# Optimization experiments

Measured on AMD Instinct MI355X. Metric: run time of the kernel, lower is better.

## Reference

```python
import jax, jax.numpy as jnp
import numpy as np
from jax import lax

IMG = 256; STRIDE = 16; FH = FW = 16; A = 9
SCALES = (32.0, 64.0, 128.0); RATIOS = (0.5, 1.0, 2.0)
N_PROP = 2000; CROP = 14
C_BB = 64


def _conv(x, w, b, stride=1, pad='SAME'):
    y = lax.conv_general_dilated(x, w, (stride, stride), pad,
                                 dimension_numbers=('NCHW', 'OIHW', 'NCHW'))
    return y + b[None, :, None, None]


def _anchors():
    s = jnp.array(SCALES, jnp.float32); r = jnp.array(RATIOS, jnp.float32)
    sr = jnp.stack(jnp.meshgrid(s, r, indexing='ij'), -1).reshape(-1, 2)  # [A,2]
    ws = sr[:, 0] * jnp.sqrt(sr[:, 1]); hs = sr[:, 0] / jnp.sqrt(sr[:, 1])
    cy = (jnp.arange(FH, dtype=jnp.float32) + 0.5) * STRIDE
    cx = (jnp.arange(FW, dtype=jnp.float32) + 0.5) * STRIDE
    cy, cx = jnp.meshgrid(cy, cx, indexing='ij')
    cy = cy[..., None]; cx = cx[..., None]  # [FH,FW,1]
    return jnp.stack([cx - ws / 2, cy - hs / 2, cx + ws / 2, cy + hs / 2], -1).reshape(-1, 4)


def _decode(deltas, anchors):
    w = anchors[:, 2] - anchors[:, 0]; h = anchors[:, 3] - anchors[:, 1]
    cx = anchors[:, 0] + 0.5 * w; cy = anchors[:, 1] + 0.5 * h
    ncx = cx + deltas[:, 0] * w; ncy = cy + deltas[:, 1] * h
    nw = w * jnp.exp(deltas[:, 2]); nh = h * jnp.exp(deltas[:, 3])
    return jnp.stack([ncx - 0.5 * nw, ncy - 0.5 * nh, ncx + 0.5 * nw, ncy + 0.5 * nh], -1)


def _clip(b):
    lim = jnp.float32(IMG - 1)
    return jnp.stack([jnp.clip(b[:, 0], 0, lim), jnp.clip(b[:, 1], 0, lim),
                      jnp.clip(b[:, 2], 0, lim), jnp.clip(b[:, 3], 0, lim)], -1)


def _nms(boxes, scores, thr):
    # greedy NMS; returns order (desc score) and keep mask in sorted order
    order = jnp.argsort(-scores)
    b = boxes[order]
    area = jnp.maximum(b[:, 2] - b[:, 0], 0) * jnp.maximum(b[:, 3] - b[:, 1], 0)
    xx1 = jnp.maximum(b[:, None, 0], b[None, :, 0]); yy1 = jnp.maximum(b[:, None, 1], b[None, :, 1])
    xx2 = jnp.minimum(b[:, None, 2], b[None, :, 2]); yy2 = jnp.minimum(b[:, None, 3], b[None, :, 3])
    inter = jnp.maximum(xx2 - xx1, 0) * jnp.maximum(yy2 - yy1, 0)
    iou = inter / (area[:, None] + area[None, :] - inter + 1e-8)
    n = boxes.shape[0]; idx = jnp.arange(n)
    def body(i, keep):
        return keep & ~(keep[i] & (iou[i] > thr) & (idx > i))
    keep = lax.fori_loop(0, n, body, jnp.ones(n, dtype=bool))
    return order, keep


def _crop_resize(feat, nboxes):
    # feat [C,FH,FW]; nboxes [N,4] normalized (y1,x1,y2,x2) -> [N,C,CROP,CROP]
    t = jnp.arange(CROP, dtype=jnp.float32) / (CROP - 1)
    def one(bx):
        y1, x1, y2, x2 = bx
        fy = (y1 + (y2 - y1) * t) * (FH - 1)
        fx = (x1 + (x2 - x1) * t) * (FW - 1)
        y0 = jnp.clip(jnp.floor(fy), 0, FH - 1).astype(jnp.int32); y1i = jnp.clip(y0 + 1, 0, FH - 1)
        x0 = jnp.clip(jnp.floor(fx), 0, FW - 1).astype(jnp.int32); x1i = jnp.clip(x0 + 1, 0, FW - 1)
        wy = (fy - y0.astype(fy.dtype))[:, None]   # [CROP,1]
        wx = (fx - x0.astype(fx.dtype))[None, :]   # [1,CROP]
        g = lambda yi, xi: feat[:, yi[:, None], xi[None, :]]  # [C,CROP,CROP]
        top = g(y0, x0) * (1 - wx) + g(y0, x1i) * wx
        bot = g(y1i, x0) * (1 - wx) + g(y1i, x1i) * wx
        return top * (1 - wy) + bot * wy
    return jax.vmap(one)(nboxes)


def _forward(x, w_bb, b_bb, w_rpn, b_rpn, w_cls, b_cls, w_box, b_box,
             w_fc1, b_fc1, w_fc2, b_fc2, w_rcls, b_rcls, w_rbox, b_rbox,
             w_m1, b_m1, w_m2, b_m2):
    anchors = _anchors()
    feat = jax.nn.relu(_conv(x, w_bb, b_bb, stride=STRIDE, pad='VALID'))  # [1,C,16,16]
    h = jax.nn.relu(_conv(feat, w_rpn, b_rpn))
    rpn_logits = _conv(h, w_cls, b_cls)[0].reshape(A, 2, FH, FW).transpose(2, 3, 0, 1).reshape(-1, 2)
    rpn_deltas = _conv(h, w_box, b_box)[0].reshape(A, 4, FH, FW).transpose(2, 3, 0, 1).reshape(-1, 4)
    scores = jax.nn.softmax(rpn_logits, -1)[:, 1]
    boxes = _clip(_decode(rpn_deltas, anchors))
    order, keep = _nms(boxes, scores, 0.5)
    n = boxes.shape[0]
    prio = jnp.where(keep, 0, 1) * n + jnp.arange(n)   # kept first, in score order
    sel = jnp.argsort(prio)[:N_PROP]
    valid = keep[sel]
    proposals = jnp.where(valid[:, None], boxes[order][sel], 0.0)  # [N_PROP,4] xyxy
    nb = jnp.stack([proposals[:, 1], proposals[:, 0], proposals[:, 3], proposals[:, 2]], -1) / (IMG - 1)
    crops = _crop_resize(feat[0], nb)                  # [N_PROP,C,14,14]
    pooled = crops.reshape(N_PROP, C_BB, 7, 2, 7, 2).max(axis=(3, 5))
    flat = pooled.reshape(N_PROP, -1)
    h1 = jax.nn.relu(flat @ w_fc1 + b_fc1)
    h2 = jax.nn.relu(h1 @ w_fc2 + b_fc2)
    rcnn_logits = h2 @ w_rcls + b_rcls                 # [N_PROP,2]
    rcnn_deltas = h2 @ w_rbox + b_rbox                 # [N_PROP,4]
    m = jax.nn.relu(_conv(crops, w_m1, b_m1))
    rcnn_masks = _conv(m, w_m2, b_m2)                  # [N_PROP,1,14,14]
    det_scores = jax.nn.softmax(rcnn_logits, -1)[:, 1]
    dets = _clip(_decode(rcnn_deltas, proposals))
    s2 = jnp.where(valid, det_scores, -1.0)
    order2, keep2 = _nms(dets, s2, 0.3)
    keep2 = keep2 & valid[order2]
    final_dets = jnp.where(keep2[:, None], dets[order2], 0.0)
    final_scores = jnp.where(keep2, det_scores[order2], 0.0)
    final_masks = jax.nn.sigmoid(rcnn_masks[order2][:, 0]) * keep2[:, None, None].astype(crops.dtype)
    return (rpn_logits, rpn_deltas, proposals, anchors, rcnn_logits, rcnn_deltas,
            rcnn_masks, final_dets, final_masks, final_scores, keep2)


def setup_inputs() -> dict:
    key = jax.random.key(0)
    ks = jax.random.split(key, 24)
    rn = lambda k, sh, s: jax.random.normal(k, sh, dtype=jnp.float32) * s
    C = C_BB
    return {
        'x': rn(ks[0], (1, 3, IMG, IMG), 1.0),
        'w_bb': rn(ks[1], (C, 3, STRIDE, STRIDE), 0.03), 'b_bb': jnp.zeros((C,), jnp.float32),
        'w_rpn': rn(ks[2], (C, C, 3, 3), 0.05), 'b_rpn': jnp.zeros((C,), jnp.float32),
        'w_cls': rn(ks[3], (2 * A, C, 1, 1), 0.05), 'b_cls': jnp.zeros((2 * A,), jnp.float32),
        'w_box': rn(ks[4], (4 * A, C, 1, 1), 0.05), 'b_box': jnp.zeros((4 * A,), jnp.float32),
        'w_fc1': rn(ks[5], (C * 7 * 7, 512), 0.02), 'b_fc1': jnp.zeros((512,), jnp.float32),
        'w_fc2': rn(ks[6], (512, 512), 0.04), 'b_fc2': jnp.zeros((512,), jnp.float32),
        'w_rcls': rn(ks[7], (512, 2), 0.05), 'b_rcls': jnp.zeros((2,), jnp.float32),
        'w_rbox': rn(ks[8], (512, 4), 0.05), 'b_rbox': jnp.zeros((4,), jnp.float32),
        'w_m1': rn(ks[9], (C, C, 3, 3), 0.05), 'b_m1': jnp.zeros((C,), jnp.float32),
        'w_m2': rn(ks[10], (1, C, 1, 1), 0.05), 'b_m2': jnp.zeros((1,), jnp.float32),
    }


def reference(x, w_bb, b_bb, w_rpn, b_rpn, w_cls, b_cls, w_box, b_box,
              w_fc1, b_fc1, w_fc2, b_fc2, w_rcls, b_rcls, w_rbox, b_rbox,
              w_m1, b_m1, w_m2, b_m2):
    return _forward(x, w_bb, b_bb, w_rpn, b_rpn, w_cls, b_cls, w_box, b_box,
                    w_fc1, b_fc1, w_fc2, b_fc2, w_rcls, b_rcls, w_rbox, b_rbox,
                    w_m1, b_m1, w_m2, b_m2)
```

## Files before the change

### kernel.cpp

```cpp
#include <hip/hip_runtime.h>
#include <math.h>

typedef unsigned long long u64;
typedef unsigned short u16;
typedef __attribute__((ext_vector_type(8))) short bf16x8;
typedef __attribute__((ext_vector_type(4))) float f32x4;
typedef __attribute__((ext_vector_type(16))) float f32x16;

#define N_ANCH 2304
#define NP     2000
#define W1     36
#define W2     32

#define O_RPN_LOGITS   0
#define O_RPN_DELTAS   4608
#define O_PROPOSALS    13824
#define O_ANCHORS      21824
#define O_RCNN_LOGITS  31040
#define O_RCNN_DELTAS  35040
#define O_RCNN_MASKS   43040
#define O_FINAL_DETS   435040
#define O_FINAL_MASKS  443040
#define O_FINAL_SCORES 835040
#define O_KEEP2        837040

__device__ __forceinline__ u16 f2bf(float f) {
    unsigned int x = __float_as_uint(f);
    unsigned int r = x + 0x7fffu + ((x >> 16) & 1u);
    return (u16)(r >> 16);
}

__global__ __launch_bounds__(256) void bb_conv(const float* __restrict__ x,
    const float* __restrict__ w, const float* __restrict__ b,
    float* __restrict__ feat, float* __restrict__ feat_tf)
{
    __shared__ __align__(16) float ws_[768];
    int c = blockIdx.x;
    for (int e = threadIdx.x; e < 192; e += 256)
        ((float4*)ws_)[e] = ((const float4*)(w + c*768))[e];
    __syncthreads();
    int fy = threadIdx.x >> 4, fx = threadIdx.x & 15;
    float acc = b[c];
    for (int ic = 0; ic < 3; ++ic)
        for (int ky = 0; ky < 16; ++ky) {
            const float* xr = x + (size_t)(ic*256 + fy*16+ky)*256 + fx*16;
            const float* wr = ws_ + ic*256 + ky*16;
            float xv[16];
            *(float4*)&xv[0]  = *(const float4*)(xr);
            *(float4*)&xv[4]  = *(const float4*)(xr+4);
            *(float4*)&xv[8]  = *(const float4*)(xr+8);
            *(float4*)&xv[12] = *(const float4*)(xr+12);
            #pragma unroll
            for (int kx = 0; kx < 16; ++kx) acc += xv[kx]*wr[kx];
        }
    float v = fmaxf(acc, 0.f);
    feat[c*256 + threadIdx.x] = v;
    feat_tf[threadIdx.x*64 + c] = v;
}

__global__ __launch_bounds__(256) void rpn_conv(const float* __restrict__ feat,
    const float* __restrict__ w, const float* __restrict__ b, float* __restrict__ h)
{
    __shared__ __align__(16) float f[16384];
    __shared__ __align__(16) float ws_[576];
    int c = blockIdx.x;
    for (int e = threadIdx.x; e < 4096; e += 256)
        ((float4*)f)[e] = ((const float4*)feat)[e];
    for (int e = threadIdx.x; e < 144; e += 256)
        ((float4*)ws_)[e] = ((const float4*)(w + c*576))[e];
    __syncthreads();
    int fy = threadIdx.x >> 4, fx = threadIdx.x & 15;
    float acc = b[c];
    for (int ic = 0; ic < 64; ++ic) {
        const float* fc = f + ic*256;
        const float* wc = ws_ + ic*9;
        #pragma unroll
        for (int dy = 0; dy < 3; ++dy) {
            int y = fy + dy - 1;
            if (y < 0 || y > 15) continue;
            #pragma unroll
            for (int dx = 0; dx < 3; ++dx) {
                int xx = fx + dx - 1;
                if (xx < 0 || xx > 15) continue;
                acc += fc[y*16+xx]*wc[dy*3+dx];
            }
        }
    }
    h[c*256 + threadIdx.x] = fmaxf(acc, 0.f);
}

__global__ __launch_bounds__(256) void heads_rpn(const float* __restrict__ hbuf,
    const float* __restrict__ w_cls, const float* __restrict__ b_cls,
    const float* __restrict__ w_box, const float* __restrict__ b_box,
    float* __restrict__ out_logits, float* __restrict__ out_deltas,
    float* __restrict__ out_anchors,
    float* __restrict__ scores, float* __restrict__ boxes)
{
    int idx = blockIdx.x*256 + threadIdx.x;
    if (idx >= N_ANCH) return;
    int fy = idx / 144, r = idx % 144, fx = r / 9, a = r % 9;
    int pix = fy*16 + fx;
    float l0 = b_cls[a*2+0], l1 = b_cls[a*2+1];
    float d0 = b_box[a*4+0], d1 = b_box[a*4+1], d2 = b_box[a*4+2], d3 = b_box[a*4+3];
    const float* wc0 = w_cls + (a*2+0)*64;
    const float* wc1 = w_cls + (a*2+1)*64;
    const float* wb0 = w_box + (a*4+0)*64;
    const float* wb1 = w_box + (a*4+1)*64;
    const float* wb2 = w_box + (a*4+2)*64;
    const float* wb3 = w_box + (a*4+3)*64;
    for (int c = 0; c < 64; ++c) {
        float hv = hbuf[c*256 + pix];
        l0 += hv*wc0[c]; l1 += hv*wc1[c];
        d0 += hv*wb0[c]; d1 += hv*wb1[c]; d2 += hv*wb2[c]; d3 += hv*wb3[c];
    }
    out_logits[idx*2+0] = l0; out_logits[idx*2+1] = l1;
    out_deltas[idx*4+0] = d0; out_deltas[idx*4+1] = d1;
    out_deltas[idx*4+2] = d2; out_deltas[idx*4+3] = d3;
    float mx = fmaxf(l0,l1);
    float e0 = expf(l0-mx), e1 = expf(l1-mx);
    scores[idx] = e1/(e0+e1);
    float SC = (a/3 == 0) ? 32.f : ((a/3 == 1) ? 64.f : 128.f);
    float RT = (a%3 == 0) ? 0.5f : ((a%3 == 1) ? 1.f : 2.f);
    float wsz = SC*sqrtf(RT), hsz = SC/sqrtf(RT);
    float cx = (fx+0.5f)*16.f, cy = (fy+0.5f)*16.f;
    float ax1 = cx - wsz*0.5f, ay1 = cy - hsz*0.5f;
    float ax2 = cx + wsz*0.5f, ay2 = cy + hsz*0.5f;
    out_anchors[idx*4+0]=ax1; out_anchors[idx*4+1]=ay1;
    out_anchors[idx*4+2]=ax2; out_anchors[idx*4+3]=ay2;
    float aw = ax2-ax1, ah = ay2-ay1;
    float acx = ax1 + 0.5f*aw, acy = ay1 + 0.5f*ah;
    float ncx = acx + d0*aw, ncy = acy + d1*ah;
    float nw = aw*expf(d2), nh = ah*expf(d3);
    float x1 = ncx - 0.5f*nw, y1 = ncy - 0.5f*nh;
    float x2 = ncx + 0.5f*nw, y2 = ncy + 0.5f*nh;
    const float lim = 255.f;
    x1 = fminf(fmaxf(x1,0.f),lim); y1 = fminf(fmaxf(y1,0.f),lim);
    x2 = fminf(fmaxf(x2,0.f),lim); y2 = fminf(fmaxf(y2,0.f),lim);
    boxes[idx*4+0]=x1; boxes[idx*4+1]=y1; boxes[idx*4+2]=x2; boxes[idx*4+3]=y2;
}

__global__ __launch_bounds__(256) void sort_rank(const float* __restrict__ score,
                                                 int* __restrict__ order, int n)
{
    __shared__ float sc[2304];
    for (int i = threadIdx.x; i < n; i += 256) sc[i] = score[i];
    __syncthreads();
    int i = blockIdx.x*256 + threadIdx.x;
    if (i >= n) return;
    float si = sc[i];
    int r = 0;
    for (int j = 0; j < n; ++j) {
        float sj = sc[j];
        r += (sj > si) || (sj == si && j < i);
    }
    order[r] = i;
}

__global__ __launch_bounds__(256) void gather_sorted(const float4* __restrict__ boxes,
    const int* __restrict__ order, float4* __restrict__ sb, float* __restrict__ sa, int n)
{
    int i = blockIdx.x*256 + threadIdx.x;
    if (i >= n) return;
    float4 b = boxes[order[i]];
    sb[i] = b;
    sa[i] = fmaxf(b.z-b.x, 0.f)*fmaxf(b.w-b.y, 0.f);
}

__global__ __launch_bounds__(256) void iou_mask(const float4* __restrict__ sb,
    const float* __restrict__ sa, int n, int ntotal, int words, float thr,
    u64* __restrict__ mask)
{
    int gid = blockIdx.x*256 + threadIdx.x;
    if (gid >= ntotal*words) return;
    int i = gid / words, w = gid % words;
    if (i >= n) { mask[(size_t)i*words + w] = 0; return; }
    float4 bi = sb[i]; float ai = sa[i];
    u64 m = 0;
    int j0 = w*64;
    for (int bb = 0; bb < 64; ++bb) {
        int j = j0 + bb;
        if (j > i && j < n) {
            float4 bj = sb[j];
            float xx1 = fmaxf(bi.x, bj.x), yy1 = fmaxf(bi.y, bj.y);
            float xx2 = fminf(bi.z, bj.z), yy2 = fminf(bi.w, bj.w);
            float inter = fmaxf(xx2-xx1, 0.f)*fmaxf(yy2-yy1, 0.f);
            float iou = inter / (ai + sa[j] - inter + 1e-8f);
            if (iou > thr) m |= 1ULL << bb;
        }
    }
    mask[(size_t)i*words + w] = m;
}

__global__ __launch_bounds__(256, 1) void nms_scan_wg(const u64* __restrict__ mask,
    int nblk, int words, u64* __restrict__ remout)
{
    __shared__ u64 rem_lds[64];
    __shared__ u64 diagS[64];
    __shared__ u64 pslot[8*64];
    int t = threadIdx.x;
    int ngrp = 256 / words;
    int g = t / words, c = t % words;
    bool pactive = (g < ngrp);
    int gg = min(g, ngrp - 1);
    if (t < 64) {
        rem_lds[t] = ~0ULL;
        diagS[t] = mask[(size_t)t*words + 0];
    }
    __syncthreads();
    for (int b = 0; b < nblk; ++b) {
        const u64* blockbase = mask + (size_t)(64*b)*words;
        u64 vals[10];
        int rows[10];
        #pragma unroll
        for (int k = 0; k < 10; ++k) {
            int r = min(gg + k*ngrp, 63);
            rows[k] = r;
            vals[k] = blockbase[(size_t)r*words + c];
        }
        u64 dnext = mask[(size_t)(64*(b+1) + (t & 63))*words + min(b+1, words-1)];
        u64 mydia = diagS[t & 63];
        u64 nz = __ballot(mydia != 0ULL);
        u64 cur = rem_lds[b];
        u64 pend = cur & nz;
        unsigned mlo = (unsigned)mydia;
        unsigned mhi = (unsigned)(mydia >> 32);
        while (pend) {
            int i = __ffsll((unsigned long long)pend) - 1;
            unsigned lo = __builtin_amdgcn_readlane((int)mlo, i);
            unsigned hi = __builtin_amdgcn_readlane((int)mhi, i);
            u64 dia = ((u64)hi << 32) | lo;
            cur  &= ~dia;
            pend &= ~dia;
            pend &= pend - 1;
        }
        u64 partial = ~0ULL;
        #pragma unroll
        for (int k = 0; k < 10; ++k) {
            bool al = (cur >> rows[k]) & 1ULL;
            partial &= al ? ~vals[k] : ~0ULL;
        }
        if (pactive) pslot[g*64 + c] = partial;
        __syncthreads();
        if (t < 64) diagS[t] = dnext;
        if (t < words) {
            u64 red = rem_lds[t];
            for (int g2 = 0; g2 < ngrp; ++g2) red &= pslot[g2*64 + t];
            rem_lds[t] = red;
        }
        __syncthreads();
    }
    if (t < words) remout[t] = rem_lds[t];
}

__global__ __launch_bounds__(256) void select_props(const u64* __restrict__ remw,
    const float4* __restrict__ sboxes, float* __restrict__ prop_out,
    float4* __restrict__ propws, int* __restrict__ validat, int* __restrict__ kcnt)
{
    __shared__ int cnt[256];
    __shared__ int pref[257];
    int t = threadIdx.x;
    int base = t*9;
    int c = 0;
    #pragma unroll
    for (int q = 0; q < 9; ++q) { int i = base+q; c += (int)((remw[i>>6]>>(i&63))&1ULL); }
    cnt[t] = c; __syncthreads();
    if (t == 0) { pref[0]=0; for (int u=0;u<256;u++) pref[u+1]=pref[u]+cnt[u]; }
    __syncthreads();
    int K = pref[256];
    if (t == 0) kcnt[0] = K;
    int kb = pref[t];
    int nb = K + (base - pref[t]);
    for (int q = 0; q < 9; ++q) {
        int i = base + q;
        int k = (int)((remw[i>>6]>>(i&63))&1ULL);
        int pos = k ? kb : nb;
        if (k) kb++; else nb++;
        if (pos < NP) {
            validat[pos] = k;
            float4 p = k ? sboxes[i] : make_float4(0.f,0.f,0.f,0.f);
            propws[pos] = p;
            prop_out[pos*4+0]=p.x; prop_out[pos*4+1]=p.y;
            prop_out[pos*4+2]=p.z; prop_out[pos*4+3]=p.w;
        }
    }
}

__global__ __launch_bounds__(256) void prep_wbt(const float* __restrict__ w, u16* __restrict__ wbt)
{
    int e = blockIdx.x*256 + threadIdx.x;
    if (e >= 36864) return;
    int oc = e / 576, rem = e % 576, ic = rem / 9, tap = rem % 9;
    int kg = ic >> 4, half = (ic >> 3) & 1, el = ic & 7;
    wbt[((tap*4 + kg)*2 + half)*512 + oc*8 + el] = f2bf(w[e]);
}

__global__ __launch_bounds__(256, 3) void mask_head_fused(const float* __restrict__ feat_tf,
    const float4* __restrict__ propws, const u16* __restrict__ wbt,
    const float* __restrict__ b_m1, const float* __restrict__ w_m2,
    const float* __restrict__ b_m2, float* __restrict__ masks_out,
    float* __restrict__ flat, const int* __restrict__ kcnt)
{
    __shared__ __align__(16) u16 crop[256*64];
    __shared__ unsigned pooled[3136];
    __shared__ __align__(16) int4 cidx[196];
    __shared__ float2 cwt[196];
    __shared__ int2 cmeta[196];
    __shared__ __align__(16) float wm2s[64];
    __shared__ __align__(16) float b1s[64];
    int n = blockIdx.x;
    if (n > *kcnt) return;
    int t = threadIdx.x;
    float4 p = propws[n];

    #pragma unroll
    for (int k = 0; k < 8; ++k)
        *(int4*)(crop + k*2048 + t*8) = make_int4(0,0,0,0);
    for (int e = t; e < 3136; e += 256) pooled[e] = 0;
    if (t < 64) { wm2s[t] = w_m2[t]; b1s[t] = b_m1[t]; }
    if (t < 196) {
        float x1n = p.x*(1.f/255.f), y1n = p.y*(1.f/255.f);
        float x2n = p.z*(1.f/255.f), y2n = p.w*(1.f/255.f);
        int py = t / 14, px = t - py*14;
        float fyv = (y1n + (y2n-y1n)*(py*(1.f/13.f)))*15.f;
        float fxv = (x1n + (x2n-x1n)*(px*(1.f/13.f)))*15.f;
        int y0 = min(max((int)floorf(fyv),0),15), y1i = min(y0+1,15);
        int x0 = min(max((int)floorf(fxv),0),15), x1i = min(x0+1,15);
        float wy = fyv - (float)y0, wx = fxv - (float)x0;
        cidx[t] = make_int4((y0*16+x0)*64, (y0*16+x1i)*64, (y1i*16+x0)*64, (y1i*16+x1i)*64);
        cwt[t] = make_float2(wy, wx);
        cmeta[t] = make_int2((py+1)*16 + px + 1, (py>>1)*7 + (px>>1));
    }
    __syncthreads();

    int wave = t >> 6, lane = t & 63;
    for (int it = 0; it < 49; ++it) {
        int idx = it*4 + wave;
        int4 o4 = cidx[idx];
        float2 w2 = cwt[idx];
        int2 mt = cmeta[idx];
        float v00 = feat_tf[o4.x + lane];
        float v01 = feat_tf[o4.y + lane];
        float v10 = feat_tf[o4.z + lane];
        float v11 = feat_tf[o4.w + lane];
        float wy = w2.x, wx = w2.y;
        float top = v00*(1.f-wx) + v01*wx;
        float bot = v10*(1.f-wx) + v11*wx;
        float val = top*(1.f-wy) + bot*wy;
        int g = mt.x;
        crop[g*64 + (((lane>>3) ^ (g&7))<<3) + (lane&7)] = f2bf(val);
        atomicMax(&pooled[lane*49 + mt.y], __float_as_uint(val));
    }
    __syncthreads();

    {
        size_t rowoff = (size_t)n*3136;
        for (int k = t; k < 3136; k += 256)
            flat[rowoff + k] = __uint_as_float(pooled[k]);
    }

    int l31 = lane & 31, half = lane >> 5;
    int pix0 = wave*64 + l31, pix1 = pix0 + 32;

    f32x16 acc[2][2];
    #pragma unroll
    for (int o = 0; o < 2; ++o) {
        #pragma unroll
        for (int q = 0; q < 4; ++q) {
            float4 b4 = *(const float4*)&b1s[o*32 + 4*half + 8*q];
            #pragma unroll
            for (int pp = 0; pp < 2; ++pp) {
                acc[pp][o][q*4+0] = b4.x; acc[pp][o][q*4+1] = b4.y;
                acc[pp][o][q*4+2] = b4.z; acc[pp][o][q*4+3] = b4.w;
            }
        }
    }

    for (int tap = 0; tap < 9; ++tap) {
        int doff = (tap/3 - 1)*16 + (tap%3) - 1;
        int p0 = (pix0 + doff) & 255;
        int p1 = (pix1 + doff) & 255;
        const u16* wt = wbt + tap*4096;
        bf16x8 af[2][4];
        #pragma unroll
        for (int kg = 0; kg < 4; ++kg) {
            #pragma unroll
            for (int o = 0; o < 2; ++o)
                af[o][kg] = *(const bf16x8*)(wt + (kg*2 + half)*512 + (o*32 + l31)*8);
        }
        int x0v = p0&7, x1v = p1&7;
        #pragma unroll
        for (int kg = 0; kg < 4; ++kg) {
            int slot = kg*2 + half;
            bf16x8 bf0 = *(const bf16x8*)(crop + p0*64 + ((slot ^ x0v)<<3));
            bf16x8 bf1 = *(const bf16x8*)(crop + p1*64 + ((slot ^ x1v)<<3));
            acc[0][0] = __builtin_amdgcn_mfma_f32_32x32x16_bf16(af[0][kg], bf0, acc[0][0], 0, 0, 0);
            acc[0][1] = __builtin_amdgcn_mfma_f32_32x32x16_bf16(af[1][kg], bf0, acc[0][1], 0, 0, 0);
            acc[1][0] = __builtin_amdgcn_mfma_f32_32x32x16_bf16(af[0][kg], bf1, acc[1][0], 0, 0, 0);
            acc[1][1] = __builtin_amdgcn_mfma_f32_32x32x16_bf16(af[1][kg], bf1, acc[1][1], 0, 0, 0);
        }
    }

    float4 wmq[2][4];
    #pragma unroll
    for (int o = 0; o < 2; ++o)
        #pragma unroll
        for (int q = 0; q < 4; ++q)
            wmq[o][q] = *(const float4*)&wm2s[o*32 + 4*half + 8*q];
    float s0 = 0.f, s1 = 0.f;
    #pragma unroll
    for (int o = 0; o < 2; ++o) {
        #pragma unroll
        for (int q = 0; q < 4; ++q) {
            float4 w4 = wmq[o][q];
            s0 = fmaf(fmaxf(acc[0][o][q*4+0], 0.f), w4.x, s0);
            s0 = fmaf(fmaxf(acc[0][o][q*4+1], 0.f), w4.y, s0);
            s0 = fmaf(fmaxf(acc[0][o][q*4+2], 0.f), w4.z, s0);
            s0 = fmaf(fmaxf(acc[0][o][q*4+3], 0.f), w4.w, s0);
            s1 = fmaf(fmaxf(acc[1][o][q*4+0], 0.f), w4.x, s1);
            s1 = fmaf(fmaxf(acc[1][o][q*4+1], 0.f), w4.y, s1);
            s1 = fmaf(fmaxf(acc[1][o][q*4+2], 0.f), w4.z, s1);
            s1 = fmaf(fmaxf(acc[1][o][q*4+3], 0.f), w4.w, s1);
        }
    }
    s0 += __shfl_xor(s0, 32);
    s1 += __shfl_xor(s1, 32);
    float sv = (half ? s1 : s0) + b_m2[0];
    int pw = half ? pix1 : pix0;
    int pyy = (pw>>4) - 1, pxx = (pw&15) - 1;
    if ((unsigned)pyy < 14u && (unsigned)pxx < 14u)
        masks_out[(size_t)n*196 + pyy*14 + pxx] = sv;
}

__global__ __launch_bounds__(256) void bcast_rows(const int* __restrict__ kcnt,
    float* __restrict__ out_logits, float* __restrict__ out_deltas,
    float* __restrict__ masks_out, float4* __restrict__ dets,
    float* __restrict__ dscores, float* __restrict__ s2)
{
    int K = *kcnt;
    int j = blockIdx.x;
    if (j <= K) return;
    int t = threadIdx.x;
    if (t < 196) {
        masks_out[(size_t)j*196 + t] = masks_out[(size_t)K*196 + t];
    } else if (t == 196) {
        out_logits[j*2+0] = out_logits[K*2+0];
        out_logits[j*2+1] = out_logits[K*2+1];
    } else if (t == 197) {
        out_deltas[j*4+0] = out_deltas[K*4+0];
        out_deltas[j*4+1] = out_deltas[K*4+1];
        out_deltas[j*4+2] = out_deltas[K*4+2];
        out_deltas[j*4+3] = out_deltas[K*4+3];
    } else if (t == 198) {
        dets[j] = dets[K];
        dscores[j] = dscores[K];
        s2[j] = s2[K];
    }
}

__global__ __launch_bounds__(128) void gemm_f32_t32(const float* __restrict__ A,
    const float* __restrict__ B, float* __restrict__ Cpart,
    int M, int N, int K, int Kblk, const int* __restrict__ kcnt)
{
    int row0 = blockIdx.x*32, col0 = blockIdx.y*64;
    if (row0 > *kcnt) return;
    __shared__ float As[32][36];
    __shared__ float Bs[32][68];
    int s = blockIdx.z;
    int kbase = s*Kblk;
    int t = threadIdx.x;

    int arow = t >> 2;
    int ak   = (t & 3) * 8;
    int am = min(row0 + arow, M-1);
    const float* Arow = A + (size_t)am*K + kbase;
    int bk = t >> 2;
    int bc = (t & 3) * 16;
    const float* Bbase = B + (size_t)(kbase + bk)*N + col0 + bc;

    int wv = t >> 6, lane = t & 63;
    int cx = lane & 15;
    int ry = lane >> 4;
    int rbase = wv*16 + ry*4;
    int cxx = cx*4;

    float4 pa0 = *(const float4*)(Arow + ak);
    float4 pa1 = *(const float4*)(Arow + ak + 4);
    float4 pb0 = *(const float4*)(Bbase);
    float4 pb1 = *(const float4*)(Bbase + 4);
    float4 pb2 = *(const float4*)(Bbase + 8);
    float4 pb3 = *(const float4*)(Bbase + 12);

    float acc[4][4] = {};
    for (int k0 = 0; k0 < Kblk; k0 += 32) {
        As[ak+0][arow]=pa0.x; As[ak+1][arow]=pa0.y; As[ak+2][arow]=pa0.z; As[ak+3][arow]=pa0.w;
        As[ak+4][arow]=pa1.x; As[ak+5][arow]=pa1.y; As[ak+6][arow]=pa1.z; As[ak+7][arow]=pa1.w;
        *(float4*)&Bs[bk][bc]    = pb0;
        *(float4*)&Bs[bk][bc+4]  = pb1;
        *(float4*)&Bs[bk][bc+8]  = pb2;
        *(float4*)&Bs[bk][bc+12] = pb3;
        __syncthreads();
        int kn = k0 + 32;
        if (kn < Kblk) {
            pa0 = *(const float4*)(Arow + kn + ak);
            pa1 = *(const float4*)(Arow + kn + ak + 4);
            pb0 = *(const float4*)(Bbase + (size_t)kn*N);
            pb1 = *(const float4*)(Bbase + (size_t)kn*N + 4);
            pb2 = *(const float4*)(Bbase + (size_t)kn*N + 8);
            pb3 = *(const float4*)(Bbase + (size_t)kn*N + 12);
        }
        #pragma unroll
        for (int k = 0; k < 32; ++k) {
            float4 av = *(float4*)&As[k][rbase];
            float4 bv = *(float4*)&Bs[k][cxx];
            float a_[4] = {av.x, av.y, av.z, av.w};
            float b_[4] = {bv.x, bv.y, bv.z, bv.w};
            #pragma unroll
            for (int i = 0; i < 4; ++i)
                #pragma unroll
                for (int j = 0; j < 4; ++j)
                    acc[i][j] = fmaf(a_[i], b_[j], acc[i][j]);
        }
        __syncthreads();
    }
    float* Cp = Cpart + (size_t)s*M*N;
    #pragma unroll
    for (int i = 0; i < 4; ++i) {
        int gm = row0 + rbase + i;
        if (gm >= M) continue;
        #pragma unroll
        for (int j = 0; j < 4; ++j) {
            int gn = col0 + cxx + j;
            Cp[(size_t)gm*N + gn] = acc[i][j];
        }
    }
}

__global__ __launch_bounds__(256) void combine_parts(const float* __restrict__ parts,
    const float* __restrict__ bias, float* __restrict__ C,
    int MN, int N, int S, int relu, const int* __restrict__ kcnt)
{
    int i4 = blockIdx.x*256 + threadIdx.x;
    if (i4*4 >= MN) return;
    size_t idx = (size_t)i4*4;
    if ((int)(idx / (unsigned)N) > *kcnt) return;
    float4 acc = *(const float4*)(parts + idx);
    for (int s = 1; s < S; ++s) {
        float4 v = *(const float4*)(parts + (size_t)s*MN + idx);
        acc.x += v.x; acc.y += v.y; acc.z += v.z; acc.w += v.w;
    }
    int nb = (int)(idx & (N-1));
    float4 bv = *(const float4*)(bias + nb);
    acc.x += bv.x; acc.y += bv.y; acc.z += bv.z; acc.w += bv.w;
    if (relu) {
        acc.x = fmaxf(acc.x, 0.f); acc.y = fmaxf(acc.y, 0.f);
        acc.z = fmaxf(acc.z, 0.f); acc.w = fmaxf(acc.w, 0.f);
    }
    *(float4*)(C + idx) = acc;
}

__global__ __launch_bounds__(256) void rcnn_heads_lds(const float* __restrict__ h2,
    const float* __restrict__ w_rcls, const float* __restrict__ b_rcls,
    const float* __restrict__ w_rbox, const float* __restrict__ b_rbox,
    const float4* __restrict__ propws, const int* __restrict__ validat,
    float* __restrict__ out_logits, float* __restrict__ out_deltas,
    float4* __restrict__ dets, float* __restrict__ dscores, float* __restrict__ s2,
    const int* __restrict__ kcnt)
{
    int b0 = blockIdx.x*8;
    if (b0 > *kcnt) return;
    __shared__ float hs[8*520];
    for (int e = threadIdx.x; e < 8*512; e += 256) {
        int pr = e >> 9, k = e & 511;
        hs[pr*520 + k] = h2[(size_t)(b0+pr)*512 + k];
    }
    __syncthreads();
    int t = threadIdx.x;
    if (t >= 8) return;
    int n = b0 + t;
    const float* hv = hs + t*520;
    float l0 = b_rcls[0], l1 = b_rcls[1];
    float d0 = b_rbox[0], d1 = b_rbox[1], d2 = b_rbox[2], d3 = b_rbox[3];
    for (int k = 0; k < 512; ++k) {
        float v = hv[k];
        l0 = fmaf(v, w_rcls[k*2+0], l0); l1 = fmaf(v, w_rcls[k*2+1], l1);
        d0 = fmaf(v, w_rbox[k*4+0], d0); d1 = fmaf(v, w_rbox[k*4+1], d1);
        d2 = fmaf(v, w_rbox[k*4+2], d2); d3 = fmaf(v, w_rbox[k*4+3], d3);
    }
    out_logits[n*2+0]=l0; out_logits[n*2+1]=l1;
    out_deltas[n*4+0]=d0; out_deltas[n*4+1]=d1;
    out_deltas[n*4+2]=d2; out_deltas[n*4+3]=d3;
    float mx = fmaxf(l0,l1);
    float e0 = expf(l0-mx), e1 = expf(l1-mx);
    float sc = e1/(e0+e1);
    float4 p = propws[n];
    float w = p.z-p.x, h = p.w-p.y;
    float cx = p.x + 0.5f*w, cy = p.y + 0.5f*h;
    float ncx = cx + d0*w, ncy = cy + d1*h;
    float nw = w*expf(d2), nh = h*expf(d3);
    float x1 = ncx-0.5f*nw, y1 = ncy-0.5f*nh, x2 = ncx+0.5f*nw, y2 = ncy+0.5f*nh;
    const float lim = 255.f;
    x1 = fminf(fmaxf(x1,0.f),lim); y1 = fminf(fmaxf(y1,0.f),lim);
    x2 = fminf(fmaxf(x2,0.f),lim); y2 = fminf(fmaxf(y2,0.f),lim);
    dets[n] = make_float4(x1,y1,x2,y2);
    dscores[n] = sc;
    s2[n] = validat[n] ? sc : -1.0f;
}

__global__ void finalize(const u64* __restrict__ remw2,
    const int* __restrict__ order2, const int* __restrict__ validat,
    const float4* __restrict__ dets, const float* __restrict__ dscores,
    const float* __restrict__ masks_in, float* __restrict__ fdets,
    float* __restrict__ fscores, float* __restrict__ fmasks, float* __restrict__ keep2out)
{
    int j = blockIdx.x;
    int t = threadIdx.x;
    int o = order2[j];
    int kb = (int)((remw2[j>>6] >> (j&63)) & 1ULL);
    int k2 = kb & validat[o];
    if (t == 0) {
        float4 d = dets[o];
        if (!k2) d = make_float4(0.f,0.f,0.f,0.f);
        fdets[j*4+0]=d.x; fdets[j*4+1]=d.y; fdets[j*4+2]=d.z; fdets[j*4+3]=d.w;
        fscores[j] = k2 ? dscores[o] : 0.f;
        keep2out[j] = (float)k2;
    }
    if (t < 196) {
        float mv = masks_in[(size_t)o*196 + t];
        float sg = 1.f/(1.f + expf(-mv));
        fmasks[(size_t)j*196 + t] = k2 ? sg : 0.f;
    }
}

extern "C" void kernel_launch(void* const* d_in, const int* in_sizes, int n_in,
                              void* d_out, int out_size, void* d_ws, size_t ws_size,
                              hipStream_t stream)
{
    const float* x      = (const float*)d_in[0];
    const float* w_bb   = (const float*)d_in[1];
    const float* b_bb   = (const float*)d_in[2];
    const float* w_rpn  = (const float*)d_in[3];
    const float* b_rpn  = (const float*)d_in[4];
    const float* w_cls  = (const float*)d_in[5];
    const float* b_cls  = (const float*)d_in[6];
    const float* w_box  = (const float*)d_in[7];
    const float* b_box  = (const float*)d_in[8];
    const float* w_fc1  = (const float*)d_in[9];
    const float* b_fc1  = (const float*)d_in[10];
    const float* w_fc2  = (const float*)d_in[11];
    const float* b_fc2  = (const float*)d_in[12];
    const float* w_rcls = (const float*)d_in[13];
    const float* b_rcls = (const float*)d_in[14];
    const float* w_rbox = (const float*)d_in[15];
    const float* b_rbox = (const float*)d_in[16];
    const float* w_m1   = (const float*)d_in[17];
    const float* b_m1   = (const float*)d_in[18];
    const float* w_m2   = (const float*)d_in[19];
    const float* b_m2   = (const float*)d_in[20];

    float* out = (float*)d_out;

    char* basep = (char*)d_ws;
    auto alloc = [&](size_t bytes) { char* q = basep; basep += (bytes + 255) & ~(size_t)255; return q; };
    float* feat    = (float*)alloc(16384*4);
    float* feat_tf = (float*)alloc(16384*4);
    float* hbuf    = (float*)alloc(16384*4);
    float* scores  = (float*)alloc(2304*4);
    float* boxes   = (float*)alloc(9216*4);
    int*   order1  = (int*)  alloc(2304*4);
    float* sboxes  = (float*)alloc(9216*4);
    float* sareas  = (float*)alloc(2304*4);
    u64*   supm1   = (u64*)  alloc((size_t)((W1+1)*64)*W1*8);
    u64*   remw1   = (u64*)  alloc(W1*8);
    int*   validat = (int*)  alloc(NP*4);
    float* propws  = (float*)alloc(NP*4*4);
    int*   kcnt    = (int*)  alloc(4);
    u16*   wbt     = (u16*)  alloc(36864*2);
    float* flat    = (float*)alloc((size_t)NP*3136*4);
    float* h1      = (float*)alloc((size_t)NP*512*4);
    float* h2      = (float*)alloc((size_t)NP*512*4);
    float* gparts  = (float*)alloc((size_t)7*NP*512*4);
    float* dets    = (float*)alloc(NP*4*4);
    float* dscores = (float*)alloc(NP*4);
    float* s2      = (float*)alloc(NP*4);
    int*   order2  = (int*)  alloc(NP*4);
    float* sdets   = (float*)alloc(NP*4*4);
    float* sareas2 = (float*)alloc(NP*4);
    u64*   supm2   = (u64*)  alloc((size_t)((W2+1)*64)*W2*8);
    u64*   remw2   = (u64*)  alloc(W2*8);

    bb_conv<<<64, 256, 0, stream>>>(x, w_bb, b_bb, feat, feat_tf);
    rpn_conv<<<64, 256, 0, stream>>>(feat, w_rpn, b_rpn, hbuf);
    heads_rpn<<<9, 256, 0, stream>>>(hbuf, w_cls, b_cls, w_box, b_box,
        out + O_RPN_LOGITS, out + O_RPN_DELTAS, out + O_ANCHORS, scores, boxes);

    sort_rank<<<9, 256, 0, stream>>>(scores, order1, N_ANCH);
    gather_sorted<<<9, 256, 0, stream>>>((const float4*)boxes, order1,
                                         (float4*)sboxes, sareas, N_ANCH);
    iou_mask<<<(W1*64*W1+255)/256, 256, 0, stream>>>((const float4*)sboxes, sareas,
                                                     N_ANCH, W1*64, W1, 0.5f, supm1);
    nms_scan_wg<<<1, 256, 0, stream>>>(supm1, W1, W1, remw1);
    select_props<<<1, 256, 0, stream>>>(remw1, (const float4*)sboxes,
                                        out + O_PROPOSALS, (float4*)propws, validat, kcnt);

    prep_wbt<<<144, 256, 0, stream>>>(w_m1, wbt);

    mask_head_fused<<<NP, 256, 0, stream>>>(feat_tf, (const float4*)propws, wbt,
        b_m1, w_m2, b_m2, out + O_RCNN_MASKS, flat, kcnt);
    gemm_f32_t32<<<dim3(63, 8, 7), 128, 0, stream>>>(flat, w_fc1, gparts,
                                                     NP, 512, 3136, 448, kcnt);
    combine_parts<<<(NP*512/4+255)/256, 256, 0, stream>>>(gparts, b_fc1, h1,
                                                          NP*512, 512, 7, 1, kcnt);
    gemm_f32_t32<<<dim3(63, 8, 2), 128, 0, stream>>>(h1, w_fc2, gparts,
                                                     NP, 512, 512, 256, kcnt);
    combine_parts<<<(NP*512/4+255)/256, 256, 0, stream>>>(gparts, b_fc2, h2,
                                                          NP*512, 512, 2, 1, kcnt);
    rcnn_heads_lds<<<250, 256, 0, stream>>>(h2, w_rcls, b_rcls, w_rbox, b_rbox,
        (const float4*)propws, validat, out + O_RCNN_LOGITS, out + O_RCNN_DELTAS,
        (float4*)dets, dscores, s2, kcnt);

    bcast_rows<<<NP, 256, 0, stream>>>(kcnt, out + O_RCNN_LOGITS, out + O_RCNN_DELTAS,
        out + O_RCNN_MASKS, (float4*)dets, dscores, s2);

    sort_rank<<<8, 256, 0, stream>>>(s2, order2, NP);
    gather_sorted<<<8, 256, 0, stream>>>((const float4*)dets, order2,
                                         (float4*)sdets, sareas2, NP);
    iou_mask<<<(W2*64*W2+255)/256, 256, 0, stream>>>((const float4*)sdets, sareas2,
                                                     NP, W2*64, W2, 0.3f, supm2);
    nms_scan_wg<<<1, 256, 0, stream>>>(supm2, W2, W2, remw2);
    finalize<<<NP, 256, 0, stream>>>(remw2, order2, validat, (const float4*)dets,
        dscores, out + O_RCNN_MASKS, out + O_FINAL_DETS, out + O_FINAL_SCORES,
        out + O_FINAL_MASKS, out + O_KEEP2);
}
```

Baseline: 537.6 us.

## Split rank sort into 2D partial-count kernel plus scatter reduction

Replaces the single-pass rank sort (9 or 8 blocks, each thread scanning all n scores) with a 2D grid where each block counts against a 256-score tile, then a second kernel sums the partial counts and scatters. This raises parallelism from 9 to 81 blocks and vectorizes the LDS reads with float4. It adds an extra kernel launch and a partial-count buffer round trip through global memory.

```diff
diff --git a/kernel.cpp b/kernel.cpp
--- a/kernel.cpp
+++ b/kernel.cpp
@@ -139,20 +139,40 @@
     boxes[idx*4+0]=x1; boxes[idx*4+1]=y1; boxes[idx*4+2]=x2; boxes[idx*4+3]=y2;
 }
 
-__global__ __launch_bounds__(256) void sort_rank(const float* __restrict__ score,
-                                                 int* __restrict__ order, int n)
-{
-    __shared__ float sc[2304];
-    for (int i = threadIdx.x; i < n; i += 256) sc[i] = score[i];
+__global__ __launch_bounds__(256) void rank_part(const float* __restrict__ score,
+    int* __restrict__ parts, int n)
+{
+    __shared__ __align__(16) float sj[256];
+    int it = blockIdx.x, jt = blockIdx.y;
+    int i = it*256 + threadIdx.x;
+    int j0 = jt*256;
+    int jj = j0 + threadIdx.x;
+    sj[threadIdx.x] = (jj < n) ? score[jj] : 0.f;
     __syncthreads();
+    if (i >= n) return;
+    float si = score[i];
+    int jmax = min(256, n - j0);
+    int cnt = 0;
+    const float4* s4 = (const float4*)sj;
+    int q4 = jmax >> 2;
+    for (int q = 0; q < q4; ++q) {
+        float4 v = s4[q];
+        int j = j0 + q*4;
+        cnt += (v.x > si) || (v.x == si && (j+0) < i);
+        cnt += (v.y > si) || (v.y == si && (j+1) < i);
+        cnt += (v.z > si) || (v.z == si && (j+2) < i);
+        cnt += (v.w > si) || (v.w == si && (j+3) < i);
+    }
+    parts[(size_t)jt*n + i] = cnt;
+}
+
+__global__ __launch_bounds__(256) void rank_scatter(const int* __restrict__ parts,
+    int* __restrict__ order, int n, int S)
+{
     int i = blockIdx.x*256 + threadIdx.x;
     if (i >= n) return;
-    float si = sc[i];
     int r = 0;
-    for (int j = 0; j < n; ++j) {
-        float sj = sc[j];
-        r += (sj > si) || (sj == si && j < i);
-    }
+    for (int s = 0; s < S; ++s) r += parts[(size_t)s*n + i];
     order[r] = i;
 }
 
@@ -667,6 +687,7 @@
     float* scores  = (float*)alloc(2304*4);
     float* boxes   = (float*)alloc(9216*4);
     int*   order1  = (int*)  alloc(2304*4);
+    int*   rparts  = (int*)  alloc((size_t)9*2304*4);
     float* sboxes  = (float*)alloc(9216*4);
     float* sareas  = (float*)alloc(2304*4);
     u64*   supm1   = (u64*)  alloc((size_t)((W1+1)*64)*W1*8);
@@ -693,7 +714,8 @@
     heads_rpn<<<9, 256, 0, stream>>>(hbuf, w_cls, b_cls, w_box, b_box,
         out + O_RPN_LOGITS, out + O_RPN_DELTAS, out + O_ANCHORS, scores, boxes);
 
-    sort_rank<<<9, 256, 0, stream>>>(scores, order1, N_ANCH);
+    rank_part<<<dim3(9, 9), 256, 0, stream>>>(scores, rparts, N_ANCH);
+    rank_scatter<<<9, 256, 0, stream>>>(rparts, order1, N_ANCH, 9);
     gather_sorted<<<9, 256, 0, stream>>>((const float4*)boxes, order1,
                                          (float4*)sboxes, sareas, N_ANCH);
     iou_mask<<<(W1*64*W1+255)/256, 256, 0, stream>>>((const float4*)sboxes, sareas,
@@ -721,7 +743,8 @@
     bcast_rows<<<NP, 256, 0, stream>>>(kcnt, out + O_RCNN_LOGITS, out + O_RCNN_DELTAS,
         out + O_RCNN_MASKS, (float4*)dets, dscores, s2);
 
-    sort_rank<<<8, 256, 0, stream>>>(s2, order2, NP);
+    rank_part<<<dim3(8, 8), 256, 0, stream>>>(s2, rparts, NP);
+    rank_scatter<<<8, 256, 0, stream>>>(rparts, order2, NP, 8);
     gather_sorted<<<8, 256, 0, stream>>>((const float4*)dets, order2,
                                          (float4*)sdets, sareas2, NP);
     iou_mask<<<(W2*64*W2+255)/256, 256, 0, stream>>>((const float4*)sdets, sareas2,
```

Measured after the change: 448.3 us. 1.2x faster.
